# Optimization experiments

Measured on AMD Instinct MI355X. Metric: run time of the kernel, lower is better.

The kernel has to match this reference:

```python
import jax, jax.numpy as jnp
import numpy as np

# Production-scale dims: total AST nodes, total CFG nodes, number of mapping pairs
N_AST, N_CFG, M = 500_000, 100_000, 400_000
D_AST, D_CFG = 256, 256


def setup_inputs() -> dict:
    key = jax.random.key(0)
    ks = jax.random.split(key, 6)
    prev = jax.random.normal(ks[0], (N_AST, D_AST), jnp.float32)
    cfg = jax.random.normal(ks[1], (N_CFG, D_CFG), jnp.float32)
    # unique key indices (a random subset of AST node ids) -> deterministic scatter
    key_indices = jax.random.permutation(ks[2], N_AST)[:M].astype(jnp.int32)
    value_indices = jax.random.randint(ks[3], (M,), 0, N_CFG, jnp.int32)
    s_u = 1.0 / np.sqrt(D_CFG)
    W_update = jax.random.uniform(ks[4], (D_CFG, D_AST), jnp.float32, -s_u, s_u)
    b_update = jnp.zeros((D_AST,), jnp.float32)
    s_g = 1.0 / np.sqrt(2 * D_AST)
    W_gate = jax.random.uniform(ks[5], (2 * D_AST, D_AST), jnp.float32, -s_g, s_g)
    b_gate = jnp.zeros((D_AST,), jnp.float32)
    return dict(
        previous_ast_nodes_encodings=prev,
        new_cfg_nodes_encodings=cfg,
        key_indices=key_indices,
        value_indices=value_indices,
        W_update=W_update,
        b_update=b_update,
        W_gate=W_gate,
        b_gate=b_gate,
    )


def reference(previous_ast_nodes_encodings, new_cfg_nodes_encodings,
              key_indices, value_indices, W_update, b_update, W_gate, b_gate):
    # gather: rows of AST-node state and CFG-node updates participating in the mapping
    state = previous_ast_nodes_encodings[key_indices]      # [M, D_AST]
    upd = new_cfg_nodes_encodings[value_indices]           # [M, D_CFG]
    # StateUpdater (gated update; dropout is identity in eval mode)
    proj = jax.nn.relu(upd @ W_update + b_update)          # project update to state dim
    gate = jax.nn.sigmoid(jnp.concatenate([state, proj], axis=-1) @ W_gate + b_gate)
    new_state = gate * state + (1.0 - gate) * proj         # [M, D_AST]
    # scatter updated rows back into the full AST-node encodings tensor
    return previous_ast_nodes_encodings.at[key_indices].set(new_state)
```

## Files before the change

### kernel.cpp

```cpp
#include <hip/hip_runtime.h>
#include <hip/hip_bf16.h>

typedef __attribute__((ext_vector_type(8))) short short8;
typedef __attribute__((ext_vector_type(4))) float f32x4;
typedef __attribute__((ext_vector_type(4))) unsigned short u16x4;

#define D 256

static __device__ __forceinline__ unsigned short f2bf(float f) {
    union { __hip_bfloat16 h; unsigned short u; } v;
    v.h = __float2bfloat16(f);
    return v.u;
}
static __device__ __forceinline__ float bf2f(unsigned short h) {
    union { unsigned u; float f; } v; v.u = ((unsigned)h) << 16;
    return v.f;
}

__global__ void pack_w_kernel(const float* __restrict__ W, unsigned short* __restrict__ dst,
                              int log2nkk, int total) {
    int p = blockIdx.x * blockDim.x + threadIdx.x;
    if (p >= total) return;
    int j     = p & 7;
    int lane  = (p >> 3) & 63;
    int kk    = (p >> 9) & ((1 << log2nkk) - 1);
    int ntile = p >> (9 + log2nkk);
    int k = kk * 32 + ((lane >> 4) * 8) + j;
    int n = ntile * 16 + (lane & 15);
    dst[p] = f2bf(W[k * D + n]);
}

__global__ void clear_flags_kernel(unsigned* __restrict__ f, int n) {
    int i = blockIdx.x * blockDim.x + threadIdx.x;
    if (i < n) f[i] = 0u;
}

__global__ void scatter_flags_kernel(const int* __restrict__ kidx,
                                     unsigned char* __restrict__ flags, int m) {
    int i = blockIdx.x * blockDim.x + threadIdx.x;
    if (i < m) flags[kidx[i]] = 1;
}

__global__ void copy_rows_kernel(const f32x4* __restrict__ src, f32x4* __restrict__ dst,
                                 const unsigned char* __restrict__ flags, int nrows) {
    int w    = (blockIdx.x * blockDim.x + threadIdx.x) >> 6;
    int lane = threadIdx.x & 63;
    int nw   = (gridDim.x * blockDim.x) >> 6;
    for (int row = w; row < nrows; row += nw) {
        if (flags[row]) continue;
        size_t idx = (size_t)row * 64 + lane;
        f32x4 v = __builtin_nontemporal_load(src + idx);
        __builtin_nontemporal_store(v, dst + idx);
    }
}

__global__ __launch_bounds__(256, 5) void projall_kernel(
    const float* __restrict__ cfg, const unsigned short* __restrict__ WuP,
    const float* __restrict__ bu, unsigned short* __restrict__ projall, int ncfg)
{
    __shared__ unsigned short Aub[64 * D];
    char* aubB = (char*)Aub;
    const int t = threadIdx.x, lane = t & 63, wid = t >> 6;
    const int lr = lane & 15, lk = lane >> 4;
    const int base = blockIdx.x * 64;

    #pragma unroll
    for (int i = 0; i < 16; ++i) {
        int row = wid * 16 + i;
        int r = base + row;
        f32x4 u = (f32x4){0.f, 0.f, 0.f, 0.f};
        if (r < ncfg) u = *(const f32x4*)(cfg + (size_t)r * D + lane * 4);
        int boff = (lane * 8) ^ ((row & 7) << 4);
        u16x4 hu;
        hu.x = f2bf(u.x); hu.y = f2bf(u.y); hu.z = f2bf(u.z); hu.w = f2bf(u.w);
        *(u16x4*)(aubB + row * 512 + boff) = hu;
    }
    __syncthreads();

    f32x4 acc[4][4];
    #pragma unroll
    for (int fm = 0; fm < 4; ++fm)
        #pragma unroll
        for (int fn = 0; fn < 4; ++fn)
            acc[fm][fn] = (f32x4){0.f, 0.f, 0.f, 0.f};

    #pragma unroll
    for (int kk = 0; kk < 8; ++kk) {
        short8 a[4], b[4];
        #pragma unroll
        for (int fm = 0; fm < 4; ++fm) {
            int row = fm * 16 + lr;
            int boff = (kk * 64 + lk * 16) ^ ((row & 7) << 4);
            a[fm] = *(const short8*)(aubB + row * 512 + boff);
        }
        #pragma unroll
        for (int fn = 0; fn < 4; ++fn) {
            int ntile = wid * 4 + fn;
            b[fn] = *(const short8*)(WuP + ((size_t)(ntile * 8 + kk) * 64 + lane) * 8);
        }
        #pragma unroll
        for (int fm = 0; fm < 4; ++fm)
            #pragma unroll
            for (int fn = 0; fn < 4; ++fn)
                acc[fm][fn] = __builtin_amdgcn_mfma_f32_16x16x32_bf16(a[fm], b[fn], acc[fm][fn], 0, 0, 0);
    }

    float bu4[4];
    #pragma unroll
    for (int fn = 0; fn < 4; ++fn) bu4[fn] = bu[wid * 64 + fn * 16 + lr];

    #pragma unroll
    for (int fm = 0; fm < 4; ++fm) {
        #pragma unroll
        for (int i = 0; i < 4; ++i) {
            int r = base + fm * 16 + lk * 4 + i;
            if (r >= ncfg) continue;
            #pragma unroll
            for (int fn = 0; fn < 4; ++fn) {
                float p = acc[fm][fn][i] + bu4[fn];
                p = p > 0.f ? p : 0.f;
                projall[(size_t)r * D + wid * 64 + fn * 16 + lr] = f2bf(p);
            }
        }
    }
}

__global__ __launch_bounds__(512, 4) void fused2_kernel(
    const float* __restrict__ prev, const unsigned short* __restrict__ projall,
    const int* __restrict__ kidx, const int* __restrict__ vidx,
    const unsigned short* __restrict__ WgP, const float* __restrict__ bg,
    float* __restrict__ out)
{
    __shared__ unsigned short Ast[64 * D];
    __shared__ unsigned short Apj[64 * D];
    char* astB = (char*)Ast;
    char* apjB = (char*)Apj;

    const int t    = threadIdx.x;
    const int lane = t & 63;
    const int wid  = t >> 6;
    const int lr   = lane & 15;
    const int lk   = lane >> 4;
    const int base = blockIdx.x * 64;

    #pragma unroll
    for (int i = 0; i < 8; ++i) {
        int row = wid * 8 + i;
        int kr = kidx[base + row];
        f32x4 s = __builtin_nontemporal_load((const f32x4*)(prev + (size_t)kr * D) + lane);
        int boff = (lane * 8) ^ ((row & 7) << 4);
        u16x4 hs;
        hs.x = f2bf(s.x); hs.y = f2bf(s.y); hs.z = f2bf(s.z); hs.w = f2bf(s.w);
        *(u16x4*)(astB + row * 512 + boff) = hs;
    }
    #pragma unroll
    for (int i = 0; i < 4; ++i) {
        int row = wid * 8 + i * 2 + (lane >> 5);
        int vr = vidx[base + row];
        short8 pv = *(const short8*)(projall + (size_t)vr * D + (lane & 31) * 8);
        int boff = ((lane & 31) * 16) ^ ((row & 7) << 4);
        *(short8*)(apjB + row * 512 + boff) = pv;
    }
    __syncthreads();

    f32x4 acc2[4][2];
    #pragma unroll
    for (int fm = 0; fm < 4; ++fm)
        #pragma unroll
        for (int fn = 0; fn < 2; ++fn)
            acc2[fm][fn] = (f32x4){0.f, 0.f, 0.f, 0.f};

    #pragma unroll
    for (int kk = 0; kk < 16; ++kk) {
        const char* Asrc = (kk < 8) ? astB : apjB;
        int kkl = kk & 7;
        short8 a[4], b[2];
        #pragma unroll
        for (int fm = 0; fm < 4; ++fm) {
            int row = fm * 16 + lr;
            int boff = (kkl * 64 + lk * 16) ^ ((row & 7) << 4);
            a[fm] = *(const short8*)(Asrc + row * 512 + boff);
        }
        #pragma unroll
        for (int fn = 0; fn < 2; ++fn) {
            int ntile = wid * 2 + fn;
            b[fn] = *(const short8*)(WgP + ((size_t)(ntile * 16 + kk) * 64 + lane) * 8);
        }
        #pragma unroll
        for (int fm = 0; fm < 4; ++fm)
            #pragma unroll
            for (int fn = 0; fn < 2; ++fn)
                acc2[fm][fn] = __builtin_amdgcn_mfma_f32_16x16x32_bf16(a[fm], b[fn], acc2[fm][fn], 0, 0, 0);
    }

    float bg2[2];
    #pragma unroll
    for (int fn = 0; fn < 2; ++fn) bg2[fn] = bg[wid * 32 + fn * 16 + lr];

    #pragma unroll
    for (int fm = 0; fm < 4; ++fm) {
        #pragma unroll
        for (int i = 0; i < 4; ++i) {
            int row = fm * 16 + lk * 4 + i;
            int kr = kidx[base + row];
            float* orow = out + (size_t)kr * D;
            #pragma unroll
            for (int fn = 0; fn < 2; ++fn) {
                int col = wid * 32 + fn * 16 + lr;
                float x = acc2[fm][fn][i] + bg2[fn];
                float g = 1.f / (1.f + __expf(-x));
                int boff = (col * 2) ^ ((row & 7) << 4);
                float st = bf2f(*(const unsigned short*)(astB + row * 512 + boff));
                float pj = bf2f(*(const unsigned short*)(apjB + row * 512 + boff));
                orow[col] = g * st + (1.f - g) * pj;
            }
        }
    }
}

extern "C" void kernel_launch(void* const* d_in, const int* in_sizes, int n_in,
                              void* d_out, int out_size, void* d_ws, size_t ws_size,
                              hipStream_t stream) {
    const float* prev = (const float*)d_in[0];
    const float* cfg  = (const float*)d_in[1];
    const int* kidx   = (const int*)d_in[2];
    const int* vidx   = (const int*)d_in[3];
    const float* Wu   = (const float*)d_in[4];
    const float* bu   = (const float*)d_in[5];
    const float* Wg   = (const float*)d_in[6];
    const float* bg   = (const float*)d_in[7];
    float* out = (float*)d_out;

    const int N_AST = in_sizes[0] / D;
    const int N_CFG = in_sizes[1] / D;
    const int M     = in_sizes[2];

    unsigned short* WuP = (unsigned short*)d_ws;
    unsigned short* WgP = WuP + 256 * 256;
    unsigned char* flags = (unsigned char*)(WgP + 512 * 256);
    unsigned short* projall = (unsigned short*)((char*)d_ws + (1 << 20));

    const int totalWu = 256 * 256;
    const int totalWg = 512 * 256;
    const int nflag4  = (N_AST + 3) / 4;

    pack_w_kernel<<<(totalWu + 255) / 256, 256, 0, stream>>>(Wu, WuP, 3, totalWu);
    pack_w_kernel<<<(totalWg + 255) / 256, 256, 0, stream>>>(Wg, WgP, 4, totalWg);
    clear_flags_kernel<<<(nflag4 + 255) / 256, 256, 0, stream>>>((unsigned*)flags, nflag4);
    scatter_flags_kernel<<<(M + 255) / 256, 256, 0, stream>>>(kidx, flags, M);

    projall_kernel<<<(N_CFG + 63) / 64, 256, 0, stream>>>(cfg, WuP, bu, projall, N_CFG);
    fused2_kernel<<<M / 64, 512, 0, stream>>>(prev, projall, kidx, vidx, WgP, bg, out);
    copy_rows_kernel<<<2048, 256, 0, stream>>>((const f32x4*)prev, (f32x4*)out, flags, N_AST);
}
```

Measured before the change: 427.2 us.

## Merge unmapped-row copy into fused gate kernel via interleaved copy blocks

The separate copy kernel for untouched rows is folded into the fused gather/GEMM/scatter kernel. Every eighth block is a copy block whose waves stream unflagged rows, so the memory-bound copy can overlap with the compute-heavy gate tiles and one launch is removed. Output stores in the gate epilogue become nontemporal, and launch bounds drop to 2 blocks per CU. Copy blocks hold the same LDS allocation as compute blocks, which may limit occupancy, and the copy work may end up unevenly balanced against the compute tiles.

After: 722.6 us. 69.1% more time.

```diff
diff --git a/kernel.cpp b/kernel.cpp
--- a/kernel.cpp
+++ b/kernel.cpp
@@ -41,19 +41,6 @@
     if (i < m) flags[kidx[i]] = 1;
 }
 
-__global__ void copy_rows_kernel(const f32x4* __restrict__ src, f32x4* __restrict__ dst,
-                                 const unsigned char* __restrict__ flags, int nrows) {
-    int w    = (blockIdx.x * blockDim.x + threadIdx.x) >> 6;
-    int lane = threadIdx.x & 63;
-    int nw   = (gridDim.x * blockDim.x) >> 6;
-    for (int row = w; row < nrows; row += nw) {
-        if (flags[row]) continue;
-        size_t idx = (size_t)row * 64 + lane;
-        f32x4 v = __builtin_nontemporal_load(src + idx);
-        __builtin_nontemporal_store(v, dst + idx);
-    }
-}
-
 __global__ __launch_bounds__(256, 5) void projall_kernel(
     const float* __restrict__ cfg, const unsigned short* __restrict__ WuP,
     const float* __restrict__ bu, unsigned short* __restrict__ projall, int ncfg)
@@ -125,23 +112,41 @@
     }
 }
 
-__global__ __launch_bounds__(512, 4) void fused2_kernel(
+__global__ __launch_bounds__(512, 2) void fused2m_kernel(
     const float* __restrict__ prev, const unsigned short* __restrict__ projall,
     const int* __restrict__ kidx, const int* __restrict__ vidx,
     const unsigned short* __restrict__ WgP, const float* __restrict__ bg,
-    float* __restrict__ out)
+    float* __restrict__ out, const unsigned char* __restrict__ flags,
+    int ntiles, int nrows, int ncopywaves)
 {
     __shared__ unsigned short Ast[64 * D];
     __shared__ unsigned short Apj[64 * D];
     char* astB = (char*)Ast;
     char* apjB = (char*)Apj;
 
-    const int t    = threadIdx.x;
-    const int lane = t & 63;
-    const int wid  = t >> 6;
+    const int bid  = blockIdx.x;
+    const int tid  = threadIdx.x;
+    const int lane = tid & 63;
+    const int wid  = tid >> 6;
+
+    if ((bid & 7) == 7) {
+        int cwave = (bid >> 3) * 8 + wid;
+        const f32x4* src = (const f32x4*)prev;
+        f32x4* dst = (f32x4*)out;
+        for (int row = cwave; row < nrows; row += ncopywaves) {
+            if (flags[row]) continue;
+            size_t idx = (size_t)row * 64 + lane;
+            f32x4 v = __builtin_nontemporal_load(src + idx);
+            __builtin_nontemporal_store(v, dst + idx);
+        }
+        return;
+    }
+
+    const int tile = bid - (bid >> 3);
+    if (tile >= ntiles) return;
+    const int base = tile * 64;
     const int lr   = lane & 15;
     const int lk   = lane >> 4;
-    const int base = blockIdx.x * 64;
 
     #pragma unroll
     for (int i = 0; i < 8; ++i) {
@@ -212,7 +217,7 @@
                 int boff = (col * 2) ^ ((row & 7) << 4);
                 float st = bf2f(*(const unsigned short*)(astB + row * 512 + boff));
                 float pj = bf2f(*(const unsigned short*)(apjB + row * 512 + boff));
-                orow[col] = g * st + (1.f - g) * pj;
+                __builtin_nontemporal_store(g * st + (1.f - g) * pj, orow + col);
             }
         }
     }
@@ -243,6 +248,12 @@
     const int totalWu = 256 * 256;
     const int totalWg = 512 * 256;
     const int nflag4  = (N_AST + 3) / 4;
+    const int ntiles  = M / 64;
+
+    int total_blocks = (ntiles * 8 + 6) / 7;
+    while (total_blocks - (total_blocks >> 3) < ntiles) ++total_blocks;
+    const int ncopy = total_blocks >> 3;
+    const int ncopywaves = ncopy * 8;
 
     pack_w_kernel<<<(totalWu + 255) / 256, 256, 0, stream>>>(Wu, WuP, 3, totalWu);
     pack_w_kernel<<<(totalWg + 255) / 256, 256, 0, stream>>>(Wg, WgP, 4, totalWg);
@@ -250,6 +261,6 @@
     scatter_flags_kernel<<<(M + 255) / 256, 256, 0, stream>>>(kidx, flags, M);
 
     projall_kernel<<<(N_CFG + 63) / 64, 256, 0, stream>>>(cfg, WuP, bu, projall, N_CFG);
-    fused2_kernel<<<M / 64, 512, 0, stream>>>(prev, projall, kidx, vidx, WgP, bg, out);
-    copy_rows_kernel<<<2048, 256, 0, stream>>>((const f32x4*)prev, (f32x4*)out, flags, N_AST);
-}
+    fused2m_kernel<<<total_blocks, 512, 0, stream>>>(prev, projall, kidx, vidx, WgP, bg,
+                                                     out, flags, ntiles, N_AST, ncopywaves);
+}
```

## Fuse unmapped-row copy into gated-update kernel and widen blocks to 1024 threads

Applied to the files above, without the earlier changes.

Removes the separate copy_rows kernel and has each gated-update block also copy a contiguous slice of unflagged rows from prev to out after its GEMM epilogue. Blocks grow from 512 to 1024 threads, so each wave computes one 16-column tile instead of two, and output stores become nontemporal. This saves one launch and lets the copy traffic overlap with the MFMA work of other blocks. In exchange it adds per-block tail work and changes register and occupancy pressure; launch_bounds(1024,8) asks for very high occupancy that the 64 KB of LDS per block may not allow.

Result: faster. 397.2 us (-7.0%).

```diff
diff --git a/kernel.cpp b/kernel.cpp
--- a/kernel.cpp
+++ b/kernel.cpp
@@ -41,19 +41,6 @@
     if (i < m) flags[kidx[i]] = 1;
 }
 
-__global__ void copy_rows_kernel(const f32x4* __restrict__ src, f32x4* __restrict__ dst,
-                                 const unsigned char* __restrict__ flags, int nrows) {
-    int w    = (blockIdx.x * blockDim.x + threadIdx.x) >> 6;
-    int lane = threadIdx.x & 63;
-    int nw   = (gridDim.x * blockDim.x) >> 6;
-    for (int row = w; row < nrows; row += nw) {
-        if (flags[row]) continue;
-        size_t idx = (size_t)row * 64 + lane;
-        f32x4 v = __builtin_nontemporal_load(src + idx);
-        __builtin_nontemporal_store(v, dst + idx);
-    }
-}
-
 __global__ __launch_bounds__(256, 5) void projall_kernel(
     const float* __restrict__ cfg, const unsigned short* __restrict__ WuP,
     const float* __restrict__ bu, unsigned short* __restrict__ projall, int ncfg)
@@ -125,27 +112,28 @@
     }
 }
 
-__global__ __launch_bounds__(512, 4) void fused2_kernel(
+__global__ __launch_bounds__(1024, 8) void fused4_kernel(
     const float* __restrict__ prev, const unsigned short* __restrict__ projall,
     const int* __restrict__ kidx, const int* __restrict__ vidx,
     const unsigned short* __restrict__ WgP, const float* __restrict__ bg,
-    float* __restrict__ out)
+    float* __restrict__ out, const unsigned char* __restrict__ flags,
+    int nrows, int rpb)
 {
     __shared__ unsigned short Ast[64 * D];
     __shared__ unsigned short Apj[64 * D];
     char* astB = (char*)Ast;
     char* apjB = (char*)Apj;
 
-    const int t    = threadIdx.x;
-    const int lane = t & 63;
-    const int wid  = t >> 6;
+    const int tid  = threadIdx.x;
+    const int lane = tid & 63;
+    const int wid  = tid >> 6;
     const int lr   = lane & 15;
     const int lk   = lane >> 4;
     const int base = blockIdx.x * 64;
 
     #pragma unroll
-    for (int i = 0; i < 8; ++i) {
-        int row = wid * 8 + i;
+    for (int i = 0; i < 4; ++i) {
+        int row = wid * 4 + i;
         int kr = kidx[base + row];
         f32x4 s = __builtin_nontemporal_load((const f32x4*)(prev + (size_t)kr * D) + lane);
         int boff = (lane * 8) ^ ((row & 7) << 4);
@@ -154,8 +142,8 @@
         *(u16x4*)(astB + row * 512 + boff) = hs;
     }
     #pragma unroll
-    for (int i = 0; i < 4; ++i) {
-        int row = wid * 8 + i * 2 + (lane >> 5);
+    for (int i = 0; i < 2; ++i) {
+        int row = wid * 4 + i * 2 + (lane >> 5);
         int vr = vidx[base + row];
         short8 pv = *(const short8*)(projall + (size_t)vr * D + (lane & 31) * 8);
         int boff = ((lane & 31) * 16) ^ ((row & 7) << 4);
@@ -163,39 +151,30 @@
     }
     __syncthreads();
 
-    f32x4 acc2[4][2];
+    f32x4 acc2[4];
     #pragma unroll
     for (int fm = 0; fm < 4; ++fm)
-        #pragma unroll
-        for (int fn = 0; fn < 2; ++fn)
-            acc2[fm][fn] = (f32x4){0.f, 0.f, 0.f, 0.f};
+        acc2[fm] = (f32x4){0.f, 0.f, 0.f, 0.f};
 
     #pragma unroll
     for (int kk = 0; kk < 16; ++kk) {
         const char* Asrc = (kk < 8) ? astB : apjB;
         int kkl = kk & 7;
-        short8 a[4], b[2];
+        short8 a[4], b;
         #pragma unroll
         for (int fm = 0; fm < 4; ++fm) {
             int row = fm * 16 + lr;
             int boff = (kkl * 64 + lk * 16) ^ ((row & 7) << 4);
             a[fm] = *(const short8*)(Asrc + row * 512 + boff);
         }
-        #pragma unroll
-        for (int fn = 0; fn < 2; ++fn) {
-            int ntile = wid * 2 + fn;
-            b[fn] = *(const short8*)(WgP + ((size_t)(ntile * 16 + kk) * 64 + lane) * 8);
-        }
+        b = *(const short8*)(WgP + ((size_t)(wid * 16 + kk) * 64 + lane) * 8);
         #pragma unroll
         for (int fm = 0; fm < 4; ++fm)
-            #pragma unroll
-            for (int fn = 0; fn < 2; ++fn)
-                acc2[fm][fn] = __builtin_amdgcn_mfma_f32_16x16x32_bf16(a[fm], b[fn], acc2[fm][fn], 0, 0, 0);
-    }
-
-    float bg2[2];
-    #pragma unroll
-    for (int fn = 0; fn < 2; ++fn) bg2[fn] = bg[wid * 32 + fn * 16 + lr];
+            acc2[fm] = __builtin_amdgcn_mfma_f32_16x16x32_bf16(a[fm], b, acc2[fm], 0, 0, 0);
+    }
+
+    const float bg1 = bg[wid * 16 + lr];
+    const int col = wid * 16 + lr;
 
     #pragma unroll
     for (int fm = 0; fm < 4; ++fm) {
@@ -203,18 +182,22 @@
         for (int i = 0; i < 4; ++i) {
             int row = fm * 16 + lk * 4 + i;
             int kr = kidx[base + row];
-            float* orow = out + (size_t)kr * D;
-            #pragma unroll
-            for (int fn = 0; fn < 2; ++fn) {
-                int col = wid * 32 + fn * 16 + lr;
-                float x = acc2[fm][fn][i] + bg2[fn];
-                float g = 1.f / (1.f + __expf(-x));
-                int boff = (col * 2) ^ ((row & 7) << 4);
-                float st = bf2f(*(const unsigned short*)(astB + row * 512 + boff));
-                float pj = bf2f(*(const unsigned short*)(apjB + row * 512 + boff));
-                orow[col] = g * st + (1.f - g) * pj;
-            }
-        }
+            float x = acc2[fm][i] + bg1;
+            float g = 1.f / (1.f + __expf(-x));
+            int boff = (col * 2) ^ ((row & 7) << 4);
+            float st = bf2f(*(const unsigned short*)(astB + row * 512 + boff));
+            float pj = bf2f(*(const unsigned short*)(apjB + row * 512 + boff));
+            __builtin_nontemporal_store(g * st + (1.f - g) * pj, out + (size_t)kr * D + col);
+        }
+    }
+
+    int start = blockIdx.x * rpb;
+    int end = start + rpb; if (end > nrows) end = nrows;
+    for (int row = start + wid; row < end; row += 16) {
+        if (flags[row]) continue;
+        size_t idx = (size_t)row * 64 + lane;
+        f32x4 v = __builtin_nontemporal_load((const f32x4*)prev + idx);
+        __builtin_nontemporal_store(v, (f32x4*)out + idx);
     }
 }
 
@@ -243,6 +226,8 @@
     const int totalWu = 256 * 256;
     const int totalWg = 512 * 256;
     const int nflag4  = (N_AST + 3) / 4;
+    const int ntiles  = M / 64;
+    const int rpb     = (N_AST + ntiles - 1) / ntiles;
 
     pack_w_kernel<<<(totalWu + 255) / 256, 256, 0, stream>>>(Wu, WuP, 3, totalWu);
     pack_w_kernel<<<(totalWg + 255) / 256, 256, 0, stream>>>(Wg, WgP, 4, totalWg);
@@ -250,6 +235,6 @@
     scatter_flags_kernel<<<(M + 255) / 256, 256, 0, stream>>>(kidx, flags, M);
 
     projall_kernel<<<(N_CFG + 63) / 64, 256, 0, stream>>>(cfg, WuP, bu, projall, N_CFG);
-    fused2_kernel<<<M / 64, 512, 0, stream>>>(prev, projall, kidx, vidx, WgP, bg, out);
-    copy_rows_kernel<<<2048, 256, 0, stream>>>((const f32x4*)prev, (f32x4*)out, flags, N_AST);
-}
+    fused4_kernel<<<ntiles, 1024, 0, stream>>>(prev, projall, kidx, vidx, WgP, bg,
+                                               out, flags, N_AST, rpb);
+}
```
